# Performance work log

Hardware: AMD Instinct MI355X
Metric: run time of the kernel (lower is better)

The kernel has to match this reference:

```python
import jax, jax.numpy as jnp
import numpy as np

NEG_SLOPE = 0.01  # torch LeakyReLU default

def leaky_relu(x):
    return jnp.where(x >= 0, x, NEG_SLOPE * x)

def gcn_conv(h, W, b, src, dst, n):
    # PyG GCNConv: linear (no bias), add self-loops, symmetric norm, scatter-add, + bias
    h = h @ W  # [N, F]
    loop = jnp.arange(n, dtype=src.dtype)
    s = jnp.concatenate([src, loop])
    d = jnp.concatenate([dst, loop])
    deg = jax.ops.segment_sum(jnp.ones_like(d, dtype=h.dtype), d, num_segments=n)
    dinv = jnp.where(deg > 0, deg ** -0.5, 0.0)
    norm = dinv[s] * dinv[d]  # [E+N]
    msg = h[s] * norm[:, None]
    out = jax.ops.segment_sum(msg, d, num_segments=n)
    return out + b

def setup_inputs() -> dict:
    key = jax.random.key(0)
    ks = jax.random.split(key, 12)
    N, E, D_IN, D_H, D_OUT, C = 100000, 3200000, 512, 128, 64, 2
    def lin(k, fi, fo):
        bound = 1.0 / np.sqrt(fi)
        k1, k2 = jax.random.split(k)
        W = jax.random.uniform(k1, (fi, fo), jnp.float32, -bound, bound)
        b = jax.random.uniform(k2, (fo,), jnp.float32, -bound, bound)
        return W, b
    W1, b1 = lin(ks[0], D_IN, D_H)
    W2, b2 = lin(ks[1], D_H, D_OUT)
    Wg1, bg1 = lin(ks[2], D_OUT, D_OUT)
    Wg2, bg2 = lin(ks[3], D_OUT, D_OUT)
    Wc, bc = lin(ks[4], D_OUT, C)
    x = jax.random.normal(ks[5], (N, D_IN), jnp.float32)
    edge_index = jax.random.randint(ks[6], (2, E), 0, N, jnp.int32)
    return {"x": x, "edge_index": edge_index, "W1": W1, "b1": b1, "W2": W2, "b2": b2,
            "Wg1": Wg1, "bg1": bg1, "Wg2": Wg2, "bg2": bg2, "Wc": Wc, "bc": bc}

def reference(x, edge_index, W1, b1, W2, b2, Wg1, bg1, Wg2, bg2, Wc, bc):
    n = x.shape[0]
    src, dst = edge_index[0], edge_index[1]
    # encoder (dropout = identity in eval)
    h = leaky_relu(x @ W1 + b1)
    h = leaky_relu(h @ W2 + b2)
    # two GCN layers
    h = leaky_relu(gcn_conv(h, Wg1, bg1, src, dst, n))
    h = leaky_relu(gcn_conv(h, Wg2, bg2, src, dst, n))
    logits = h @ Wc + bc
    return logits, h
```

## Files before the change

### kernel.cpp

```cpp
#include <hip/hip_runtime.h>
#include <hip/hip_bf16.h>

typedef __bf16 v8bf16 __attribute__((ext_vector_type(8)));
typedef float  v4f32  __attribute__((ext_vector_type(4)));
typedef unsigned short ushort8v __attribute__((ext_vector_type(8)));

static __device__ __forceinline__ float leaky(float v) { return v >= 0.0f ? v : 0.01f * v; }
static __device__ __forceinline__ float bfbits2f(unsigned short b) {
    union { unsigned u; float f; } c; c.u = ((unsigned)b) << 16; return c.f;
}
static __device__ __forceinline__ unsigned short f2bfbits(float f) {
    __hip_bfloat16 h = __float2bfloat16(f);
    unsigned short s; __builtin_memcpy(&s, &h, 2); return s;
}

constexpr int EPB  = 6400;
constexpr int BCAP = 16384;

static __device__ __forceinline__ bool role_split(int bid, int nA, int tot,
                                                  int& idxA, int& idxB) {
    const long long s0 = (long long)bid * nA / tot;
    const long long s1 = (long long)(bid + 1) * nA / tot;
    if (s1 > s0) { idxA = (int)s0; idxB = 0; return true; }
    idxA = 0; idxB = bid - (int)s0; return false;
}

__global__ __launch_bounds__(256) void prep_all(
    const float* __restrict__ W1, const float* __restrict__ W2,
    const float* __restrict__ Wg1, const float* __restrict__ Wg2,
    __hip_bfloat16* __restrict__ W1f, __hip_bfloat16* __restrict__ W2t,
    __hip_bfloat16* __restrict__ Wg1t, __hip_bfloat16* __restrict__ Wg2t,
    unsigned* __restrict__ bcur, int DIN, int DH, int DO, int NB) {
    const int fragTotal  = DIN * DH;
    const int fragBlocks = (fragTotal + 255) / 256;
    const int n2 = DH * DO, ng = DO * DO;
    const int smallTotal  = n2 + 2 * ng;
    const int smallBlocks = (smallTotal + 255) / 256;
    const int bid = blockIdx.x;
    if (bid < fragBlocks) {
        int tid = bid * 256 + threadIdx.x;
        if (tid >= fragTotal) return;
        int j = tid & 7, l = (tid >> 3) & 63, G = tid >> 9;
        int m = l & 15, q = l >> 4;
        int t = G & 7, kk = G >> 3;
        int n = t * 16 + m;
        int k = kk * 32 + q * 8 + j;
        W1f[tid] = __float2bfloat16(W1[k * DH + n]);
    } else if (bid < fragBlocks + smallBlocks) {
        int i = (bid - fragBlocks) * 256 + threadIdx.x;
        if (i < n2) {
            int r = i / DO, c = i % DO;
            W2t[c * DH + r] = __float2bfloat16(W2[i]);
        } else if (i < n2 + ng) {
            int j = i - n2; int r = j / DO, c = j % DO;
            Wg1t[c * DO + r] = __float2bfloat16(Wg1[j]);
        } else if (i < smallTotal) {
            int j = i - n2 - ng; int r = j / DO, c = j % DO;
            Wg2t[c * DO + r] = __float2bfloat16(Wg2[j]);
        }
    } else {
        int i = (bid - fragBlocks - smallBlocks) * 256 + threadIdx.x;
        if (i < NB) bcur[i] = 0u;
    }
}

struct ScatterSmem {
    unsigned stg[EPB];
    unsigned hist[512], inc[512], cur[512], start[512];
};

static __device__ __forceinline__ void scatter_body(
    int bid, ScatterSmem& sm, const int* __restrict__ src, const int* __restrict__ dst,
    unsigned* __restrict__ bcur, unsigned* __restrict__ ebuck, int E, int NB) {
    const int tid = threadIdx.x;
    sm.hist[tid] = 0u;
    __syncthreads();
    const int beg = bid * EPB;
    const int end = min(beg + EPB, E);
    unsigned myd[13];
#pragma unroll
    for (int i = 0; i < 13; i++) {
        const int e = beg + tid + i * 512;
        if (e < end) {
            const unsigned d = (unsigned)dst[e];
            myd[i] = d;
            atomicAdd(&sm.hist[d >> 8], 1u);
        }
    }
    __syncthreads();
    const unsigned h = sm.hist[tid];
    sm.inc[tid] = h;
    __syncthreads();
    for (int off = 1; off < 512; off <<= 1) {
        unsigned t = (tid >= off) ? sm.inc[tid - off] : 0u;
        __syncthreads();
        sm.inc[tid] += t;
        __syncthreads();
    }
    sm.cur[tid] = sm.inc[tid] - h;
    if (tid < NB && h > 0u)
        sm.start[tid] = (unsigned)tid * BCAP + atomicAdd(&bcur[tid], h);
    __syncthreads();
#pragma unroll
    for (int i = 0; i < 13; i++) {
        const int e = beg + tid + i * 512;
        if (e < end) {
            const unsigned b = myd[i] >> 8;
            const unsigned r = atomicAdd(&sm.cur[b], 1u);
            sm.stg[r] = (unsigned)e;
        }
    }
    __syncthreads();
    const int cnt = end - beg;
    for (int s = tid; s < cnt; s += 512) {
        const unsigned e = sm.stg[s];
        const unsigned d = (unsigned)dst[e];
        const unsigned b = d >> 8;
        const unsigned excl = sm.inc[b] - sm.hist[b];
        const unsigned pos = sm.start[b] + ((unsigned)s - excl);
        ebuck[pos] = (unsigned)src[e] | ((d & 255u) << 20);
    }
}

static __device__ __forceinline__ void enc1_body(
    int bid, uint4 (*lds)[1024], const float* __restrict__ A, const uint4* __restrict__ Bp,
    const float* __restrict__ bias, __hip_bfloat16* __restrict__ C, int M) {
    constexpr int K = 512;
    const int tid = threadIdx.x;
    const int wid = tid >> 6, lane = tid & 63;
    const int m = lane & 15, q = lane >> 4;
    const int row0 = bid * 128 + wid * 16;
    const int rowA = row0 + m;
    const int rowAc = rowA < M ? rowA : M - 1;
    const float* Ap = A + (size_t)rowAc * K + q * 8;

    v4f32 acc[8];
#pragma unroll
    for (int t = 0; t < 8; t++) acc[t] = (v4f32){0.f, 0.f, 0.f, 0.f};

    float4 ab[2][4];
    auto loadA = [&](int c, int par) {
#pragma unroll
        for (int j = 0; j < 4; j++)
            ab[par][j] = *reinterpret_cast<const float4*>(Ap + c * 64 + (j >> 1) * 32 + (j & 1) * 4);
    };
    auto stage = [&](int c, int par) {
        lds[par][tid]       = Bp[c * 1024 + tid];
        lds[par][512 + tid] = Bp[c * 1024 + 512 + tid];
    };

    stage(0, 0);
    loadA(0, 0);
    for (int c = 0; c < 8; c++) {
        __syncthreads();
        if (c < 7) { stage(c + 1, (c + 1) & 1); loadA(c + 1, (c + 1) & 1); }
        const int par = c & 1;
#pragma unroll
        for (int kk2 = 0; kk2 < 2; kk2++) {
            float4 f0 = ab[par][kk2 * 2], f1 = ab[par][kk2 * 2 + 1];
            v8bf16 a = {(__bf16)f0.x, (__bf16)f0.y, (__bf16)f0.z, (__bf16)f0.w,
                        (__bf16)f1.x, (__bf16)f1.y, (__bf16)f1.z, (__bf16)f1.w};
#pragma unroll
            for (int t = 0; t < 8; t++) {
                v8bf16 b = reinterpret_cast<const v8bf16*>(lds[par])[(kk2 * 8 + t) * 64 + lane];
                acc[t] = __builtin_amdgcn_mfma_f32_16x16x32_bf16(a, b, acc[t], 0, 0, 0);
            }
        }
    }

#pragma unroll
    for (int r = 0; r < 4; r++) {
        const int row = row0 + q * 4 + r;
        if (row >= M) continue;
#pragma unroll
        for (int t = 0; t < 8; t++) {
            const int col = t * 16 + m;
            C[(size_t)row * 128 + col] = __float2bfloat16(leaky(acc[t][r] + bias[col]));
        }
    }
}

__global__ __launch_bounds__(512, 4) void mega_scatter_enc1(
    const int* __restrict__ src, const int* __restrict__ dst,
    unsigned* __restrict__ bcur, unsigned* __restrict__ ebuck, int E, int NB, int nScatter,
    const float* __restrict__ A, const uint4* __restrict__ Bp,
    const float* __restrict__ bias, __hip_bfloat16* __restrict__ C, int M) {
    union Smem {
        ScatterSmem sc;
        uint4 g[2][1024];
    };
    __shared__ Smem sm;
    int ia, ib;
    if (role_split(blockIdx.x, nScatter, gridDim.x, ia, ib))
        scatter_body(ia, sm.sc, src, dst, bcur, ebuck, E, NB);
    else
        enc1_body(ib, sm.g, A, Bp, bias, C, M);
}

template <int NT, int MODE>
static __device__ __forceinline__ void gemm_body(
    int bid, const __hip_bfloat16* __restrict__ A, const __hip_bfloat16* __restrict__ Bt,
    const float* __restrict__ bias, const float* __restrict__ dinv,
    __hip_bfloat16* __restrict__ Cbf, int M, int K) {
    const int wid  = threadIdx.x >> 6;
    const int lane = threadIdx.x & 63;
    const int row0 = (bid * 4 + wid) << 4;
    if (row0 >= M) return;
    const int m = lane & 15, q = lane >> 4;

    const __hip_bfloat16* Ab = A + (size_t)(row0 + m) * K + q * 8;

    v4f32 acc[NT];
#pragma unroll
    for (int t = 0; t < NT; t++) acc[t] = (v4f32){0.f, 0.f, 0.f, 0.f};

    for (int k0 = 0; k0 < K; k0 += 32) {
        v8bf16 a = *reinterpret_cast<const v8bf16*>(Ab + k0);
#pragma unroll
        for (int t = 0; t < NT; t++) {
            v8bf16 b = *reinterpret_cast<const v8bf16*>(Bt + (size_t)(t * 16 + m) * K + k0 + q * 8);
            acc[t] = __builtin_amdgcn_mfma_f32_16x16x32_bf16(a, b, acc[t], 0, 0, 0);
        }
    }

    const int N = NT * 16;
#pragma unroll
    for (int r = 0; r < 4; r++) {
        const int row = row0 + q * 4 + r;
        float di = (MODE == 1) ? dinv[row] : 1.0f;
#pragma unroll
        for (int t = 0; t < NT; t++) {
            const int col = t * 16 + m;
            float v = acc[t][r];
            if (MODE == 0) v = leaky(v + bias[col]);
            else           v *= di;
            Cbf[(size_t)row * N + col] = __float2bfloat16(v);
        }
    }
}

template <int NT, int MODE>
__global__ __launch_bounds__(256) void gemm_kernel(
    const __hip_bfloat16* __restrict__ A, const __hip_bfloat16* __restrict__ Bt,
    const float* __restrict__ bias, const float* __restrict__ dinv,
    __hip_bfloat16* __restrict__ Cbf, int M, int K) {
    gemm_body<NT, MODE>(blockIdx.x, A, Bt, bias, dinv, Cbf, M, K);
}

static __device__ __forceinline__ void csr_body(
    int k, unsigned* hist, unsigned* cur, const unsigned* __restrict__ bcur,
    const unsigned* __restrict__ ebuck, uint2* __restrict__ rp2,
    float* __restrict__ dinv, int* __restrict__ csr, int NN) {
    const int tid = threadIdx.x;
    const unsigned cntb = bcur[k];
    const unsigned base = (unsigned)k * BCAP;
    const unsigned* eb = ebuck + base;
    hist[tid] = 0u;
    __syncthreads();
    for (unsigned e = tid; e < cntb; e += 256)
        atomicAdd(&hist[eb[e] >> 20], 1u);
    __syncthreads();
    const unsigned h = hist[tid];
    cur[tid] = h;
    __syncthreads();
    for (int off = 1; off < 256; off <<= 1) {
        unsigned t = (tid >= off) ? cur[tid - off] : 0u;
        __syncthreads();
        cur[tid] += t;
        __syncthreads();
    }
    const unsigned excl = cur[tid] - h;
    const int node = k * 256 + tid;
    if (node < NN) {
        rp2[node] = make_uint2(base + excl, base + excl + h);
        dinv[node] = rsqrtf((float)(h + 1u));
    }
    __syncthreads();
    cur[tid] = excl;
    __syncthreads();
    for (unsigned e = tid; e < cntb; e += 256) {
        const unsigned pk = eb[e];
        const unsigned pos = base + atomicAdd(&cur[pk >> 20], 1u);
        csr[pos] = (int)(pk & 0xFFFFFu);
    }
}

__global__ __launch_bounds__(256) void mega_csr_enc2(
    const unsigned* __restrict__ bcur, const unsigned* __restrict__ ebuck,
    uint2* __restrict__ rp2, float* __restrict__ dinv, int* __restrict__ csr,
    int NN, int nCsr,
    const __hip_bfloat16* __restrict__ A, const __hip_bfloat16* __restrict__ Bt,
    const float* __restrict__ bias, __hip_bfloat16* __restrict__ Cb, int M, int K) {
    __shared__ unsigned hist[256], cur[256];
    int ia, ib;
    if (role_split(blockIdx.x, nCsr, gridDim.x, ia, ib))
        csr_body(ia, hist, cur, bcur, ebuck, rp2, dinv, csr, NN);
    else
        gemm_body<4, 0>(ib, A, Bt, bias, nullptr, Cb, M, K);
}

template <int HEAD>
__global__ __launch_bounds__(256) void gather_kernel(
    const uint2* __restrict__ rp2, const int* __restrict__ csr_src,
    const __hip_bfloat16* __restrict__ u, const float* __restrict__ dinv,
    const float* __restrict__ bias, __hip_bfloat16* __restrict__ out_bf,
    float* __restrict__ out_h, const float* __restrict__ Wc,
    const float* __restrict__ bc, float* __restrict__ out_logits, int n) {
    const int node = blockIdx.x * 4 + (threadIdx.x >> 6);
    if (node >= n) return;
    const int lane = threadIdx.x & 63;
    const int g = lane >> 3, t = lane & 7;
    const uint2 rp = rp2[node];
    const unsigned beg = rp.x, end = rp.y;

    float s[8];
#pragma unroll
    for (int j = 0; j < 8; j++) s[j] = 0.f;

    unsigned e = beg + g;
    bool hv[4];
    int idx[4];
#pragma unroll
    for (int p = 0; p < 4; p++) {
        const unsigned ep = e + 8u * p;
        hv[p] = ep < end;
        idx[p] = hv[p] ? csr_src[ep] : 0;
    }
    while (hv[0]) {
        bool nhv[4];
        int nidx[4];
#pragma unroll
        for (int p = 0; p < 4; p++) {
            const unsigned ep = e + 32u + 8u * p;
            nhv[p] = ep < end;
            nidx[p] = nhv[p] ? csr_src[ep] : 0;
        }
        ushort8v w[4];
#pragma unroll
        for (int p = 0; p < 4; p++)
            if (hv[p]) w[p] = *reinterpret_cast<const ushort8v*>(u + (size_t)idx[p] * 64 + t * 8);
#pragma unroll
        for (int p = 0; p < 4; p++)
            if (hv[p]) {
#pragma unroll
                for (int j = 0; j < 8; j++) s[j] += bfbits2f(w[p][j]);
            }
        e += 32u;
#pragma unroll
        for (int p = 0; p < 4; p++) { hv[p] = nhv[p]; idx[p] = nidx[p]; }
    }
#pragma unroll
    for (int j = 0; j < 8; j++) {
        s[j] += __shfl_xor(s[j], 8, 64);
        s[j] += __shfl_xor(s[j], 16, 64);
        s[j] += __shfl_xor(s[j], 32, 64);
    }

    ushort8v wsr = *reinterpret_cast<const ushort8v*>(u + (size_t)node * 64 + t * 8);
#pragma unroll
    for (int j = 0; j < 8; j++) s[j] += bfbits2f(wsr[j]);

    const float di = dinv[node];
    const float4 b0 = *reinterpret_cast<const float4*>(bias + t * 8);
    const float4 b1 = *reinterpret_cast<const float4*>(bias + t * 8 + 4);
    float f[8];
    f[0] = leaky(s[0] * di + b0.x); f[1] = leaky(s[1] * di + b0.y);
    f[2] = leaky(s[2] * di + b0.z); f[3] = leaky(s[3] * di + b0.w);
    f[4] = leaky(s[4] * di + b1.x); f[5] = leaky(s[5] * di + b1.y);
    f[6] = leaky(s[6] * di + b1.z); f[7] = leaky(s[7] * di + b1.w);

    if (HEAD == 0) {
        if (g == 0) {
            ushort8v o;
#pragma unroll
            for (int j = 0; j < 8; j++) o[j] = f2bfbits(f[j]);
            *reinterpret_cast<ushort8v*>(out_bf + (size_t)node * 64 + t * 8) = o;
        }
    } else {
        if (g == 0) {
            float4 o0 = {f[0], f[1], f[2], f[3]};
            float4 o1 = {f[4], f[5], f[6], f[7]};
            *reinterpret_cast<float4*>(out_h + (size_t)node * 64 + t * 8) = o0;
            *reinterpret_cast<float4*>(out_h + (size_t)node * 64 + t * 8 + 4) = o1;
        }
        float p0 = 0.f, p1 = 0.f;
#pragma unroll
        for (int j = 0; j < 8; j++) {
            p0 += f[j] * Wc[(t * 8 + j) * 2];
            p1 += f[j] * Wc[(t * 8 + j) * 2 + 1];
        }
#pragma unroll
        for (int o = 4; o; o >>= 1) {
            p0 += __shfl_xor(p0, o, 64);
            p1 += __shfl_xor(p1, o, 64);
        }
        if (lane == 0) {
            out_logits[(size_t)node * 2 + 0] = p0 + bc[0];
            out_logits[(size_t)node * 2 + 1] = p1 + bc[1];
        }
    }
}

extern "C" void kernel_launch(void* const* d_in, const int* in_sizes, int n_in,
                              void* d_out, int out_size, void* d_ws, size_t ws_size,
                              hipStream_t stream) {
    const float* x   = (const float*)d_in[0];
    const int*   ei  = (const int*)d_in[1];
    const float* W1  = (const float*)d_in[2];
    const float* b1  = (const float*)d_in[3];
    const float* W2  = (const float*)d_in[4];
    const float* b2  = (const float*)d_in[5];
    const float* Wg1 = (const float*)d_in[6];
    const float* bg1 = (const float*)d_in[7];
    const float* Wg2 = (const float*)d_in[8];
    const float* bg2 = (const float*)d_in[9];
    const float* Wc  = (const float*)d_in[10];
    const float* bc  = (const float*)d_in[11];

    const int DH  = in_sizes[3];
    const int DIN = in_sizes[2] / DH;
    const int NN  = in_sizes[0] / DIN;
    const int E   = in_sizes[1] / 2;
    const int DO  = in_sizes[5];
    const int* src = ei;
    const int* dst = ei + E;

    char*  ws  = (char*)d_ws;
    size_t off = 0;
    auto alloc = [&](size_t bytes) {
        void* p = ws + off;
        off += (bytes + 255) & ~(size_t)255;
        return p;
    };
    const int NB = (NN + 255) >> 8;
    __hip_bfloat16* h1    = (__hip_bfloat16*)alloc((size_t)NN * DH * 2);
    __hip_bfloat16* h2    = (__hip_bfloat16*)alloc((size_t)NN * DO * 2);
    __hip_bfloat16* h3    = (__hip_bfloat16*)alloc((size_t)NN * DO * 2);
    __hip_bfloat16* ub    = (__hip_bfloat16*)alloc((size_t)NN * DO * 2);
    float*          dinv  = (float*)alloc((size_t)NN * 4);
    uint2*          rp2   = (uint2*)alloc((size_t)NN * 8);
    int*            csr   = (int*)alloc((size_t)NB * BCAP * 4);
    unsigned*       ebuck = (unsigned*)alloc((size_t)NB * BCAP * 4);
    unsigned*       bcur  = (unsigned*)alloc(512 * 4);
    __hip_bfloat16* W1f   = (__hip_bfloat16*)alloc((size_t)DIN * DH * 2);
    __hip_bfloat16* W2t   = (__hip_bfloat16*)alloc((size_t)DH * DO * 2);
    __hip_bfloat16* Wg1t  = (__hip_bfloat16*)alloc((size_t)DO * DO * 2);
    __hip_bfloat16* Wg2t  = (__hip_bfloat16*)alloc((size_t)DO * DO * 2);

    float* out_logits = (float*)d_out;
    float* out_h      = (float*)d_out + (size_t)NN * 2;

    const int fragBlocks  = (DIN * DH + 255) / 256;
    const int smallBlocks = (DH * DO + 2 * DO * DO + 255) / 256;
    const int zeroBlocks  = (NB + 255) / 256;
    prep_all<<<fragBlocks + smallBlocks + zeroBlocks, 256, 0, stream>>>(
        W1, W2, Wg1, Wg2, W1f, W2t, Wg1t, Wg2t, bcur, DIN, DH, DO, NB);

    const int nblkP = (E + EPB - 1) / EPB;
    const int enc1B = (NN + 127) / 128;
    mega_scatter_enc1<<<nblkP + enc1B, 512, 0, stream>>>(
        src, dst, bcur, ebuck, E, NB, nblkP,
        x, (const uint4*)W1f, b1, h1, NN);

    const int gemm_blocks = (NN / 16 + 3) / 4;
    mega_csr_enc2<<<NB + gemm_blocks, 256, 0, stream>>>(
        bcur, ebuck, rp2, dinv, csr, NN, NB,
        h1, W2t, b2, h2, NN, DH);

    gemm_kernel<4, 1><<<gemm_blocks, 256, 0, stream>>>(h2, Wg1t, nullptr, dinv, ub, NN, DO);
    gather_kernel<0><<<(NN + 3) / 4, 256, 0, stream>>>(rp2, csr, ub, dinv, bg1, h3,
                                                       nullptr, nullptr, nullptr, nullptr, NN);

    gemm_kernel<4, 1><<<gemm_blocks, 256, 0, stream>>>(h3, Wg2t, nullptr, dinv, ub, NN, DO);
    gather_kernel<1><<<(NN + 3) / 4, 256, 0, stream>>>(rp2, csr, ub, dinv, bg2, nullptr,
                                                       out_h, Wc, bc, out_logits, NN);
}
```

Before: 544.2 us.

## Fuse encoder layer 2 with first GCN linear and scale by dinv in gather

The second encoder GEMM and the first GCN linear transform now run back-to-back inside the CSR-build mega kernel, with the intermediate kept in LDS. This removes the h2 round trip and one kernel launch. Because dinv is not ready when that fused GEMM runs, the first gather now reads dinv per source edge and applies the scaling itself. Both gathers also process 8 edges per group per iteration instead of software-pipelining 4, which adds an extra random dinv load per edge in the first layer.

```diff
diff --git a/kernel.cpp b/kernel.cpp
--- a/kernel.cpp
+++ b/kernel.cpp
@@ -285,21 +285,84 @@
     }
 }
 
+static __device__ __forceinline__ void enc2g_body(
+    int bid, unsigned short* lds,
+    const __hip_bfloat16* __restrict__ h1, const __hip_bfloat16* __restrict__ W2t,
+    const float* __restrict__ b2, const __hip_bfloat16* __restrict__ Wg1t,
+    __hip_bfloat16* __restrict__ ubp, int M) {
+    const int wid = threadIdx.x >> 6, lane = threadIdx.x & 63;
+    const int m = lane & 15, q = lane >> 4;
+    const int row0 = bid * 64;
+    const int wrow0 = wid * 16;
+    {
+        const int rowA = row0 + wrow0 + m;
+        const int rowAc = rowA < M ? rowA : M - 1;
+        const __hip_bfloat16* Ab = h1 + (size_t)rowAc * 128 + q * 8;
+        v4f32 acc[4];
+#pragma unroll
+        for (int t = 0; t < 4; t++) acc[t] = (v4f32){0.f, 0.f, 0.f, 0.f};
+#pragma unroll
+        for (int k0 = 0; k0 < 128; k0 += 32) {
+            v8bf16 a = *reinterpret_cast<const v8bf16*>(Ab + k0);
+#pragma unroll
+            for (int t = 0; t < 4; t++) {
+                v8bf16 b = *reinterpret_cast<const v8bf16*>(W2t + (size_t)(t * 16 + m) * 128 + k0 + q * 8);
+                acc[t] = __builtin_amdgcn_mfma_f32_16x16x32_bf16(a, b, acc[t], 0, 0, 0);
+            }
+        }
+#pragma unroll
+        for (int r = 0; r < 4; r++) {
+            const int rr = wrow0 + q * 4 + r;
+#pragma unroll
+            for (int t = 0; t < 4; t++) {
+                const int cc = t * 16 + m;
+                lds[rr * 72 + cc] = f2bfbits(leaky(acc[t][r] + b2[cc]));
+            }
+        }
+    }
+    __syncthreads();
+    v4f32 acc2[4];
+#pragma unroll
+    for (int t = 0; t < 4; t++) acc2[t] = (v4f32){0.f, 0.f, 0.f, 0.f};
+#pragma unroll
+    for (int k0 = 0; k0 < 64; k0 += 32) {
+        v8bf16 a = *reinterpret_cast<const v8bf16*>(lds + (wrow0 + m) * 72 + k0 + q * 8);
+#pragma unroll
+        for (int t = 0; t < 4; t++) {
+            v8bf16 b = *reinterpret_cast<const v8bf16*>(Wg1t + (size_t)(t * 16 + m) * 64 + k0 + q * 8);
+            acc2[t] = __builtin_amdgcn_mfma_f32_16x16x32_bf16(a, b, acc2[t], 0, 0, 0);
+        }
+    }
+#pragma unroll
+    for (int r = 0; r < 4; r++) {
+        const int row = row0 + wrow0 + q * 4 + r;
+        if (row >= M) continue;
+#pragma unroll
+        for (int t = 0; t < 4; t++)
+            ubp[(size_t)row * 64 + t * 16 + m] = __float2bfloat16(acc2[t][r]);
+    }
+}
+
 __global__ __launch_bounds__(256) void mega_csr_enc2(
     const unsigned* __restrict__ bcur, const unsigned* __restrict__ ebuck,
     uint2* __restrict__ rp2, float* __restrict__ dinv, int* __restrict__ csr,
     int NN, int nCsr,
-    const __hip_bfloat16* __restrict__ A, const __hip_bfloat16* __restrict__ Bt,
-    const float* __restrict__ bias, __hip_bfloat16* __restrict__ Cb, int M, int K) {
-    __shared__ unsigned hist[256], cur[256];
+    const __hip_bfloat16* __restrict__ h1, const __hip_bfloat16* __restrict__ W2t,
+    const float* __restrict__ b2, const __hip_bfloat16* __restrict__ Wg1t,
+    __hip_bfloat16* __restrict__ ubp, int M) {
+    union SM {
+        struct { unsigned hist[256], cur[256]; } c;
+        unsigned short t[64 * 72];
+    };
+    __shared__ SM sm;
     int ia, ib;
     if (role_split(blockIdx.x, nCsr, gridDim.x, ia, ib))
-        csr_body(ia, hist, cur, bcur, ebuck, rp2, dinv, csr, NN);
+        csr_body(ia, sm.c.hist, sm.c.cur, bcur, ebuck, rp2, dinv, csr, NN);
     else
-        gemm_body<4, 0>(ib, A, Bt, bias, nullptr, Cb, M, K);
-}
-
-template <int HEAD>
+        enc2g_body(ib, sm.t, h1, W2t, b2, Wg1t, ubp, M);
+}
+
+template <int HEAD, int SCALED>
 __global__ __launch_bounds__(256) void gather_kernel(
     const uint2* __restrict__ rp2, const int* __restrict__ csr_src,
     const __hip_bfloat16* __restrict__ u, const float* __restrict__ dinv,
@@ -318,36 +381,35 @@
     for (int j = 0; j < 8; j++) s[j] = 0.f;
 
     unsigned e = beg + g;
-    bool hv[4];
-    int idx[4];
-#pragma unroll
-    for (int p = 0; p < 4; p++) {
-        const unsigned ep = e + 8u * p;
-        hv[p] = ep < end;
-        idx[p] = hv[p] ? csr_src[ep] : 0;
-    }
-    while (hv[0]) {
-        bool nhv[4];
-        int nidx[4];
-#pragma unroll
-        for (int p = 0; p < 4; p++) {
-            const unsigned ep = e + 32u + 8u * p;
-            nhv[p] = ep < end;
-            nidx[p] = nhv[p] ? csr_src[ep] : 0;
-        }
-        ushort8v w[4];
-#pragma unroll
-        for (int p = 0; p < 4; p++)
+    while (e < end) {
+        bool hv[8];
+        int idx[8];
+#pragma unroll
+        for (int p = 0; p < 8; p++) {
+            const unsigned ep = e + 8u * p;
+            hv[p] = ep < end;
+            idx[p] = hv[p] ? csr_src[ep] : 0;
+        }
+        float dv[8];
+        if (SCALED == 0) {
+#pragma unroll
+            for (int p = 0; p < 8; p++)
+                dv[p] = hv[p] ? dinv[idx[p]] : 0.f;
+        }
+        ushort8v w[8];
+#pragma unroll
+        for (int p = 0; p < 8; p++)
             if (hv[p]) w[p] = *reinterpret_cast<const ushort8v*>(u + (size_t)idx[p] * 64 + t * 8);
 #pragma unroll
-        for (int p = 0; p < 4; p++)
+        for (int p = 0; p < 8; p++)
             if (hv[p]) {
 #pragma unroll
-                for (int j = 0; j < 8; j++) s[j] += bfbits2f(w[p][j]);
+                for (int j = 0; j < 8; j++) {
+                    if (SCALED == 0) s[j] += bfbits2f(w[p][j]) * dv[p];
+                    else             s[j] += bfbits2f(w[p][j]);
+                }
             }
-        e += 32u;
-#pragma unroll
-        for (int p = 0; p < 4; p++) { hv[p] = nhv[p]; idx[p] = nidx[p]; }
+        e += 64u;
     }
 #pragma unroll
     for (int j = 0; j < 8; j++) {
@@ -356,11 +418,14 @@
         s[j] += __shfl_xor(s[j], 32, 64);
     }
 
+    const float di = dinv[node];
     ushort8v wsr = *reinterpret_cast<const ushort8v*>(u + (size_t)node * 64 + t * 8);
 #pragma unroll
-    for (int j = 0; j < 8; j++) s[j] += bfbits2f(wsr[j]);
-
-    const float di = dinv[node];
+    for (int j = 0; j < 8; j++) {
+        if (SCALED == 0) s[j] += bfbits2f(wsr[j]) * di;
+        else             s[j] += bfbits2f(wsr[j]);
+    }
+
     const float4 b0 = *reinterpret_cast<const float4*>(bias + t * 8);
     const float4 b1 = *reinterpret_cast<const float4*>(bias + t * 8 + 4);
     float f[8];
@@ -434,9 +499,8 @@
     };
     const int NB = (NN + 255) >> 8;
     __hip_bfloat16* h1    = (__hip_bfloat16*)alloc((size_t)NN * DH * 2);
-    __hip_bfloat16* h2    = (__hip_bfloat16*)alloc((size_t)NN * DO * 2);
     __hip_bfloat16* h3    = (__hip_bfloat16*)alloc((size_t)NN * DO * 2);
-    __hip_bfloat16* ub    = (__hip_bfloat16*)alloc((size_t)NN * DO * 2);
+    __hip_bfloat16* ubp   = (__hip_bfloat16*)alloc((size_t)NN * DO * 2);
     float*          dinv  = (float*)alloc((size_t)NN * 4);
     uint2*          rp2   = (uint2*)alloc((size_t)NN * 8);
     int*            csr   = (int*)alloc((size_t)NB * BCAP * 4);
@@ -462,16 +526,17 @@
         src, dst, bcur, ebuck, E, NB, nblkP,
         x, (const uint4*)W1f, b1, h1, NN);
 
+    const int encB = (NN + 63) / 64;
+    mega_csr_enc2<<<NB + encB, 256, 0, stream>>>(
+        bcur, ebuck, rp2, dinv, csr, NN, NB,
+        h1, W2t, b2, Wg1t, ubp, NN);
+
+    gather_kernel<0, 0><<<(NN + 3) / 4, 256, 0, stream>>>(rp2, csr, ubp, dinv, bg1, h3,
+                                                          nullptr, nullptr, nullptr, nullptr, NN);
+
     const int gemm_blocks = (NN / 16 + 3) / 4;
-    mega_csr_enc2<<<NB + gemm_blocks, 256, 0, stream>>>(
-        bcur, ebuck, rp2, dinv, csr, NN, NB,
-        h1, W2t, b2, h2, NN, DH);
-
-    gemm_kernel<4, 1><<<gemm_blocks, 256, 0, stream>>>(h2, Wg1t, nullptr, dinv, ub, NN, DO);
-    gather_kernel<0><<<(NN + 3) / 4, 256, 0, stream>>>(rp2, csr, ub, dinv, bg1, h3,
-                                                       nullptr, nullptr, nullptr, nullptr, NN);
-
-    gemm_kernel<4, 1><<<gemm_blocks, 256, 0, stream>>>(h3, Wg2t, nullptr, dinv, ub, NN, DO);
-    gather_kernel<1><<<(NN + 3) / 4, 256, 0, stream>>>(rp2, csr, ub, dinv, bg2, nullptr,
-                                                       out_h, Wc, bc, out_logits, NN);
-}
+    gemm_kernel<4, 1><<<gemm_blocks, 256, 0, stream>>>(h3, Wg2t, nullptr, dinv, ubp, NN, DO);
+
+    gather_kernel<1, 1><<<(NN + 3) / 4, 256, 0, stream>>>(rp2, csr, ubp, dinv, bg2, nullptr,
+                                                          out_h, Wc, bc, out_logits, NN);
+}
```

New measurement: 560.9 us. +3.1%, slower.
